# Kernel tuning notes

Hardware: AMD Instinct MI355X
Metric: run time of the kernel (lower is better)

Reference implementation:

```python
import jax, jax.numpy as jnp
import numpy as np

N, H, R, C = 50000, 16, 32, 8   # nodes, hidden, relations, classes
E = 1600000                      # edges (avg degree 32)


def setup_inputs() -> dict:
    key = jax.random.key(0)
    ks = jax.random.split(key, 6)
    edge_index = jax.random.randint(ks[0], (2, E), 0, N)
    edge_type = jax.random.randint(ks[1], (E,), 0, R)
    w1 = jax.random.normal(ks[2], (R, N, H), dtype=jnp.float32) * 0.05
    root1 = jax.random.normal(ks[3], (N, H), dtype=jnp.float32) * 0.05
    b1 = jnp.zeros((H,), jnp.float32)
    w2 = jax.random.normal(ks[4], (R, H, C), dtype=jnp.float32) * 0.05
    root2 = jax.random.normal(ks[5], (H, C), dtype=jnp.float32) * 0.05
    b2 = jnp.zeros((C,), jnp.float32)
    return {"edge_index": edge_index, "edge_type": edge_type,
            "w1": w1, "root1": root1, "b1": b1,
            "w2": w2, "root2": root2, "b2": b2}


def _rel_mean_agg(msgs, dst, edge_type, num_nodes, num_rel):
    """PyG RGCNConv aggregation: mean over edges within each (relation, target)
    pair, then sum over relations. msgs: [E, d] -> [num_nodes, d]."""
    seg = edge_type * num_nodes + dst                      # combined segment id
    tot = num_rel * num_nodes
    summed = jax.ops.segment_sum(msgs, seg, num_segments=tot)      # [R*N, d]
    cnt = jax.ops.segment_sum(jnp.ones((msgs.shape[0],), msgs.dtype), seg,
                              num_segments=tot)                    # [R*N]
    mean = summed / jnp.maximum(cnt, 1.0)[:, None]
    return mean.reshape(num_rel, num_nodes, -1).sum(axis=0)       # [N, d]


def reference(edge_index, edge_type, w1, root1, b1, w2, root2, b2):
    src, dst = edge_index[0], edge_index[1]
    # ---- layer 1: x = None -> message is weight row indexed by (rel, src)
    msgs1 = w1[edge_type, src]                             # [E, H] gather
    x = _rel_mean_agg(msgs1, dst, edge_type, N, R) + root1 + b1
    x = jax.nn.relu(x)
    # ---- layer 2: precompute per-relation transforms once: [R, N, C]
    xw = jnp.einsum('nh,rhc->rnc', x, w2)
    msgs2 = xw[edge_type, src]                             # [E, C] gather
    out = _rel_mean_agg(msgs2, dst, edge_type, N, R) + x @ root2 + b2
    return jax.nn.log_softmax(out, axis=1)
```

## Files before the change

### kernel.cpp

```cpp
#include <hip/hip_runtime.h>
#include <hip/hip_bf16.h>


constexpr int Nn = 50000;
constexpr int Hh = 16;
constexpr int Rr = 32;
constexpr int Cc = 8;
constexpr int Ee = 1600000;
constexpr int CHUNK = 4096;
constexpr int NC = (Ee + CHUNK - 1) / CHUNK;
constexpr int DSH = 7;
constexpr unsigned DLOWM = 127u;
constexpr int NBKT = (Nn + 127) / 128;
constexpr int K1 = (NC + 255) / 256;
constexpr int K2 = (NBKT + 255) / 256;
constexpr int KE = CHUNK / 256;
constexpr int SCAP = 5120;

__device__ __forceinline__ float b2f(__hip_bfloat16 v) { return __bfloat162float(v); }
__device__ __forceinline__ float bs2f(unsigned short u) {
    return __uint_as_float(((unsigned)u) << 16);
}

__global__ __launch_bounds__(256) void histA_kernel(const int* __restrict__ dst,
                                                    unsigned* __restrict__ H,
                                                    const unsigned short* __restrict__ w1s,
                                                    int* __restrict__ flag) {
    __shared__ unsigned hb[NBKT];
    int c = blockIdx.x, tid = threadIdx.x;
    if (c == 0 && tid == 0) {
        int hits = 0;
        for (int i = 0; i < 64; ++i) {
            unsigned short u = w1s[2 * i];
            int e = (u >> 7) & 0xFF;
            if (e >= 100 && e <= 130) ++hits;
        }
        *flag = (hits >= 32) ? 1 : 0;
    }
    for (int i = tid; i < NBKT; i += 256) hb[i] = 0;
    __syncthreads();
    int base = c * CHUNK;
    int n = min(CHUNK, Ee - base);
    for (int i = tid; i < n; i += 256)
        atomicAdd(&hb[((unsigned)dst[base + i]) >> DSH], 1u);
    __syncthreads();
    for (int i = tid; i < NBKT; i += 256) H[(size_t)c * NBKT + i] = hb[i];
}

__global__ __launch_bounds__(256) void scanB1_kernel(unsigned* __restrict__ H,
                                                     unsigned* __restrict__ bt) {
    __shared__ int lsum[4];
    int b = blockIdx.x, t = threadIdx.x, lane = t & 63, wv = t >> 6;
    int c0 = t * K1;
    int v[K1];
#pragma unroll
    for (int j = 0; j < K1; ++j) {
        int c = c0 + j;
        v[j] = (c < NC) ? (int)H[(size_t)c * NBKT + b] : 0;
    }
    int tot = 0;
#pragma unroll
    for (int j = 0; j < K1; ++j) { int tmp = v[j]; v[j] = tot; tot += tmp; }
    int s = tot;
#pragma unroll
    for (int o = 1; o < 64; o <<= 1) { int u = __shfl_up(s, o, 64); if (lane >= o) s += u; }
    if (lane == 63) lsum[wv] = s;
    __syncthreads();
    int basev = 0;
    for (int j = 0; j < wv; ++j) basev += lsum[j];
    int excl = basev + s - tot;
#pragma unroll
    for (int j = 0; j < K1; ++j) {
        int c = c0 + j;
        if (c < NC) H[(size_t)c * NBKT + b] = (unsigned)(excl + v[j]);
    }
    if (t == 255) bt[b] = (unsigned)(basev + s);
}

__global__ __launch_bounds__(256) void scanB2_kernel(const unsigned* __restrict__ bt,
                                                     unsigned* __restrict__ rbase) {
    __shared__ int lsum[4];
    int t = threadIdx.x, lane = t & 63, wv = t >> 6;
    int c0 = t * K2;
    int v[K2];
#pragma unroll
    for (int j = 0; j < K2; ++j) {
        int c = c0 + j;
        v[j] = (c < NBKT) ? (int)bt[c] : 0;
    }
    int tot = 0;
#pragma unroll
    for (int j = 0; j < K2; ++j) { int tmp = v[j]; v[j] = tot; tot += tmp; }
    int s = tot;
#pragma unroll
    for (int o = 1; o < 64; o <<= 1) { int u = __shfl_up(s, o, 64); if (lane >= o) s += u; }
    if (lane == 63) lsum[wv] = s;
    __syncthreads();
    int basev = 0;
    for (int j = 0; j < wv; ++j) basev += lsum[j];
    int excl = basev + s - tot;
#pragma unroll
    for (int j = 0; j < K2; ++j) {
        int c = c0 + j;
        if (c < NBKT) rbase[c] = (unsigned)(excl + v[j]);
    }
    if (t == 255) rbase[NBKT] = (unsigned)(basev + s);
}

__global__ __launch_bounds__(256) void scatC_kernel(const int* __restrict__ src,
                                                    const int* __restrict__ dst,
                                                    const int* __restrict__ et,
                                                    const unsigned* __restrict__ H,
                                                    const unsigned* __restrict__ rbase,
                                                    unsigned* __restrict__ rec) {
    __shared__ unsigned bb[NBKT];
    __shared__ unsigned hb[NBKT];
    __shared__ unsigned stg[CHUNK];
    __shared__ unsigned short bkt16[CHUNK];
    __shared__ int lsum[4];
    int c = blockIdx.x, t = threadIdx.x, lane = t & 63, wv = t >> 6;
    for (int i = t; i < NBKT; i += 256) {
        bb[i] = H[(size_t)c * NBKT + i] + rbase[i];
        hb[i] = 0;
    }
    __syncthreads();
    int base = c * CHUNK;
    int n = min(CHUNK, Ee - base);
    unsigned rcd[KE]; unsigned short bk[KE], rk[KE];
#pragma unroll
    for (int k = 0; k < KE; ++k) {
        int i = t + k * 256;
        if (i < n) {
            int e = base + i;
            unsigned d = (unsigned)dst[e];
            rcd[k] = (unsigned)src[e] | ((unsigned)et[e] << 16) | ((d & DLOWM) << 21);
            unsigned bkt = d >> DSH;
            bk[k] = (unsigned short)bkt;
            rk[k] = (unsigned short)atomicAdd(&hb[bkt], 1u);
        }
    }
    __syncthreads();
    {
        int c0 = t * 2;
        int v0 = (c0 < NBKT) ? (int)hb[c0] : 0;
        int v1 = (c0 + 1 < NBKT) ? (int)hb[c0 + 1] : 0;
        int pair = v0 + v1, s = pair;
#pragma unroll
        for (int o = 1; o < 64; o <<= 1) { int u = __shfl_up(s, o, 64); if (lane >= o) s += u; }
        if (lane == 63) lsum[wv] = s;
        __syncthreads();
        int basev = 0;
        for (int j = 0; j < wv; ++j) basev += lsum[j];
        int excl = basev + s - pair;
        if (c0 < NBKT) hb[c0] = (unsigned)excl;
        if (c0 + 1 < NBKT) hb[c0 + 1] = (unsigned)(excl + v0);
    }
    __syncthreads();
#pragma unroll
    for (int k = 0; k < KE; ++k) {
        int i = t + k * 256;
        if (i < n) {
            unsigned slot = hb[bk[k]] + rk[k];
            stg[slot] = rcd[k];
            bkt16[slot] = bk[k];
        }
    }
    __syncthreads();
    for (int i = t; i < n; i += 256) {
        unsigned b = bkt16[i];
        rec[bb[b] + (i - hb[b])] = stg[i];
    }
}

__global__ __launch_bounds__(256) void sortDl1_kernel(const unsigned* __restrict__ rec,
                                                      const unsigned* __restrict__ rbase,
                                                      unsigned* __restrict__ sorted,
                                                      int* __restrict__ offs,
                                                      const void* __restrict__ w1,
                                                      const void* __restrict__ root1,
                                                      const void* __restrict__ b1,
                                                      const int* __restrict__ flag,
                                                      float* __restrict__ x) {
    __shared__ unsigned cnt[128 * 33];
    __shared__ unsigned sb[128 * 33];
    __shared__ unsigned stg[SCAP];
    __shared__ unsigned dstart[129];
    __shared__ int l2s[2];
    int b = blockIdx.x, t = threadIdx.x, lane = t & 63, wv = t >> 6;
    for (int i = t; i < 128 * 33; i += 256) cnt[i] = 0;
    __syncthreads();
    unsigned rb = rbase[b], re = rbase[b + 1];
    int n = (int)(re - rb);
    for (int i = t; i < n; i += 256) {
        unsigned w = rec[rb + i];
        atomicAdd(&cnt[((w >> 21) & 127u) * 33 + ((w >> 16) & 31u)], 1u);
    }
    __syncthreads();
    int deg = 0;
    if (t < 128) {
#pragma unroll
        for (int r = 0; r < 32; ++r) {
            unsigned cc = cnt[t * 33 + r];
            sb[t * 33 + r] = (unsigned)deg;
            deg += (int)cc;
        }
    }
    int s = deg;
#pragma unroll
    for (int o = 1; o < 64; o <<= 1) { int u = __shfl_up(s, o, 64); if (lane >= o) s += u; }
    if (lane == 63 && wv < 2) l2s[wv] = s;
    __syncthreads();
    if (t < 128) {
        int excl = s - deg + (wv == 1 ? l2s[0] : 0);
        dstart[t] = (unsigned)excl;
        if (t == 127) dstart[128] = (unsigned)(excl + deg);
        int d = b * 128 + t;
        if (d <= Nn) offs[d] = (int)(rb + (unsigned)excl);
#pragma unroll
        for (int r = 0; r < 32; ++r) sb[t * 33 + r] += (unsigned)excl;
    }
    __syncthreads();
    for (int i = t; i < n; i += 256) {
        unsigned w = rec[rb + i];
        unsigned dlow = (w >> 21) & 127u, rel = (w >> 16) & 31u, sv = w & 0xFFFFu;
        int cell = (int)dlow * 33 + (int)rel;
        unsigned pos = atomicAdd(&sb[cell], 1u);
        unsigned cc = cnt[cell];
        if (cc > 2047u) cc = 2047u;
        stg[pos] = sv | (rel << 16) | (cc << 21);
    }
    __syncthreads();
    for (int i = t; i < n; i += 256) sorted[rb + i] = stg[i];
    int isbf = *flag;
    int ep = lane >> 2, hp = lane & 3;
    for (int j = 0; j < 32; ++j) {
        int dl = wv * 32 + j;
        int d = b * 128 + dl;
        if (d >= Nn) break;
        int s0 = (int)dstart[dl], s1 = (int)dstart[dl + 1];
        float a0 = 0.f, a1 = 0.f, a2 = 0.f, a3 = 0.f;
        if (isbf) {
            for (int i = s0 + ep; i < s1; i += 16) {
                unsigned p = stg[i];
                int ct = p >> 21, rel = (p >> 16) & 31, sv = p & 0xFFFF;
                float inv = __builtin_amdgcn_rcpf((float)ct);
                ushort4 v = ((const ushort4*)w1)[((size_t)rel * Nn + sv) * 4 + hp];
                a0 += inv * bs2f(v.x); a1 += inv * bs2f(v.y);
                a2 += inv * bs2f(v.z); a3 += inv * bs2f(v.w);
            }
        } else {
            for (int i = s0 + ep; i < s1; i += 16) {
                unsigned p = stg[i];
                int ct = p >> 21, rel = (p >> 16) & 31, sv = p & 0xFFFF;
                float inv = __builtin_amdgcn_rcpf((float)ct);
                float4 v = ((const float4*)w1)[((size_t)rel * Nn + sv) * 4 + hp];
                a0 += inv * v.x; a1 += inv * v.y; a2 += inv * v.z; a3 += inv * v.w;
            }
        }
#pragma unroll
        for (int o = 4; o < 64; o <<= 1) {
            a0 += __shfl_xor(a0, o, 64);
            a1 += __shfl_xor(a1, o, 64);
            a2 += __shfl_xor(a2, o, 64);
            a3 += __shfl_xor(a3, o, 64);
        }
        if (ep == 0) {
            float r0, r1, r2, r3, bb0, bb1, bb2, bb3;
            if (isbf) {
                ushort4 rv = ((const ushort4*)root1)[(size_t)d * 4 + hp];
                ushort4 bv = ((const ushort4*)b1)[hp];
                r0 = bs2f(rv.x); r1 = bs2f(rv.y); r2 = bs2f(rv.z); r3 = bs2f(rv.w);
                bb0 = bs2f(bv.x); bb1 = bs2f(bv.y); bb2 = bs2f(bv.z); bb3 = bs2f(bv.w);
            } else {
                float4 rv = ((const float4*)root1)[(size_t)d * 4 + hp];
                float4 bv = ((const float4*)b1)[hp];
                r0 = rv.x; r1 = rv.y; r2 = rv.z; r3 = rv.w;
                bb0 = bv.x; bb1 = bv.y; bb2 = bv.z; bb3 = bv.w;
            }
            float v0 = a0 + r0 + bb0, v1 = a1 + r1 + bb1;
            float v2 = a2 + r2 + bb2, v3 = a3 + r3 + bb3;
            *(float4*)(x + (size_t)d * Hh + hp * 4) =
                make_float4(v0 > 0.f ? v0 : 0.f, v1 > 0.f ? v1 : 0.f,
                            v2 > 0.f ? v2 : 0.f, v3 > 0.f ? v3 : 0.f);
        }
    }
}

__global__ __launch_bounds__(256) void l2_kernel(const unsigned* __restrict__ sorted,
                                                 const int* __restrict__ offs,
                                                 const float* __restrict__ x,
                                                 const void* __restrict__ w2,
                                                 const void* __restrict__ root2,
                                                 const void* __restrict__ b2v,
                                                 const int* __restrict__ flag,
                                                 void* __restrict__ out) {
    __shared__ float w2s[32 * 132];
    __shared__ float rsh[128];
    __shared__ float b2sh[8];
    int tid = threadIdx.x, w = tid >> 6, lane = tid & 63;
    int isbf = *flag;
    {
        int r = tid >> 3, cc = tid & 7;
        if (isbf) {
            const __hip_bfloat16* W = (const __hip_bfloat16*)w2 + r * 128 + cc;
#pragma unroll
            for (int h = 0; h < 16; ++h) w2s[r * 132 + cc * 16 + h] = b2f(W[h * 8]);
        } else {
            const float* W = (const float*)w2 + r * 128 + cc;
#pragma unroll
            for (int h = 0; h < 16; ++h) w2s[r * 132 + cc * 16 + h] = W[h * 8];
        }
    }
    if (tid < 128) rsh[tid] = isbf ? b2f(((const __hip_bfloat16*)root2)[tid])
                                   : ((const float*)root2)[tid];
    if (tid < 8)   b2sh[tid] = isbf ? b2f(((const __hip_bfloat16*)b2v)[tid])
                                    : ((const float*)b2v)[tid];
    __syncthreads();
    int ep = lane >> 3, c = lane & 7;
    int d = blockIdx.x * 4 + w;
    int off = offs[d], deg = offs[d + 1] - off;
    float acc = 0.0f;
    for (int i0 = 0; i0 < deg; i0 += 8) {
        int i = i0 + ep;
        if (i < deg) {
            unsigned p = sorted[off + i];
            int cnt = p >> 21, rel = (p >> 16) & 31, s = p & 0xFFFF;
            float inv = __builtin_amdgcn_rcpf((float)cnt);
            const float4* xr = (const float4*)(x + (size_t)s * Hh);
            float4 x0 = xr[0], x1 = xr[1], x2 = xr[2], x3 = xr[3];
            const float4* wv = (const float4*)(w2s + rel * 132 + c * 16);
            float4 w0 = wv[0], w1v = wv[1], w2v = wv[2], w3 = wv[3];
            float dot = x0.x*w0.x + x0.y*w0.y + x0.z*w0.z + x0.w*w0.w
                      + x1.x*w1v.x + x1.y*w1v.y + x1.z*w1v.z + x1.w*w1v.w
                      + x2.x*w2v.x + x2.y*w2v.y + x2.z*w2v.z + x2.w*w2v.w
                      + x3.x*w3.x + x3.y*w3.y + x3.z*w3.z + x3.w*w3.w;
            acc += inv * dot;
        }
    }
    acc += __shfl_xor(acc, 8, 64);
    acc += __shfl_xor(acc, 16, 64);
    acc += __shfl_xor(acc, 32, 64);
    if (ep == 0) {
        const float4* xr = (const float4*)(x + (size_t)d * Hh);
        float4 x0 = xr[0], x1 = xr[1], x2 = xr[2], x3 = xr[3];
        float xv[16] = {x0.x,x0.y,x0.z,x0.w, x1.x,x1.y,x1.z,x1.w,
                        x2.x,x2.y,x2.z,x2.w, x3.x,x3.y,x3.z,x3.w};
        float v = acc + b2sh[c];
#pragma unroll
        for (int h = 0; h < 16; ++h) v += xv[h] * rsh[h * 8 + c];
        float m = v;
#pragma unroll
        for (int o = 1; o < 8; o <<= 1) m = fmaxf(m, __shfl_xor(m, o, 8));
        float ssum = __expf(v - m);
#pragma unroll
        for (int o = 1; o < 8; o <<= 1) ssum += __shfl_xor(ssum, o, 8);
        float res = v - m - __logf(ssum);
        if (isbf) ((__hip_bfloat16*)out)[(size_t)d * Cc + c] = __float2bfloat16(res);
        else      ((float*)out)[(size_t)d * Cc + c] = res;
    }
}

extern "C" void kernel_launch(void* const* d_in, const int* in_sizes, int n_in,
                              void* d_out, int out_size, void* d_ws, size_t ws_size,
                              hipStream_t stream) {
    const int* edge_index = (const int*)d_in[0];
    const int* src = edge_index;
    const int* dst = edge_index + Ee;
    const int* et  = (const int*)d_in[1];
    const void* w1    = d_in[2];
    const void* root1 = d_in[3];
    const void* b1    = d_in[4];
    const void* w2    = d_in[5];
    const void* root2 = d_in[6];
    const void* b2    = d_in[7];

    unsigned* rec    = (unsigned*)d_ws;
    unsigned* sorted = rec + Ee;
    float*    x      = (float*)(sorted + Ee);
    unsigned* H      = (unsigned*)(x + (size_t)Nn * Hh);
    unsigned* bt     = H + (size_t)NC * NBKT;
    unsigned* rbase  = bt + NBKT;
    int* offs        = (int*)(rbase + NBKT + 1);
    int* flag        = offs + Nn + 4;

    histA_kernel<<<NC, 256, 0, stream>>>(dst, H, (const unsigned short*)w1, flag);
    scanB1_kernel<<<NBKT, 256, 0, stream>>>(H, bt);
    scanB2_kernel<<<1, 256, 0, stream>>>(bt, rbase);
    scatC_kernel<<<NC, 256, 0, stream>>>(src, dst, et, H, rbase, rec);
    sortDl1_kernel<<<NBKT, 256, 0, stream>>>(rec, rbase, sorted, offs,
                                             w1, root1, b1, flag, x);
    l2_kernel<<<Nn / 4, 256, 0, stream>>>(sorted, offs, x, w2, root2, b2, flag, d_out);
}
```

Measured before the change: 316.4 us.

## Replace per-destination sort with bucketed LDS atomic accumulation for both layers

```diff
diff --git a/kernel.cpp b/kernel.cpp
--- a/kernel.cpp
+++ b/kernel.cpp
@@ -9,18 +9,20 @@
 constexpr int Ee = 1600000;
 constexpr int CHUNK = 4096;
 constexpr int NC = (Ee + CHUNK - 1) / CHUNK;
-constexpr int DSH = 7;
-constexpr unsigned DLOWM = 127u;
-constexpr int NBKT = (Nn + 127) / 128;
+constexpr int DSH = 6;
+constexpr unsigned DLOWM = 63u;
+constexpr int NBKT = (Nn + 63) / 64;
 constexpr int K1 = (NC + 255) / 256;
 constexpr int K2 = (NBKT + 255) / 256;
+constexpr int KH = 4;
 constexpr int KE = CHUNK / 256;
-constexpr int SCAP = 5120;
-
-__device__ __forceinline__ float b2f(__hip_bfloat16 v) { return __bfloat162float(v); }
+constexpr unsigned SENT = 0xFFFFFFFFu;
+
 __device__ __forceinline__ float bs2f(unsigned short u) {
     return __uint_as_float(((unsigned)u) << 16);
 }
+__device__ __forceinline__ float blo(unsigned u) { return __uint_as_float(u << 16); }
+__device__ __forceinline__ float bhi(unsigned u) { return __uint_as_float(u & 0xFFFF0000u); }
 
 __global__ __launch_bounds__(256) void histA_kernel(const int* __restrict__ dst,
                                                     unsigned* __restrict__ H,
@@ -141,19 +143,29 @@
     }
     __syncthreads();
     {
-        int c0 = t * 2;
-        int v0 = (c0 < NBKT) ? (int)hb[c0] : 0;
-        int v1 = (c0 + 1 < NBKT) ? (int)hb[c0 + 1] : 0;
-        int pair = v0 + v1, s = pair;
+        int c0 = t * KH;
+        int v[KH];
+#pragma unroll
+        for (int j = 0; j < KH; ++j) {
+            int cc = c0 + j;
+            v[j] = (cc < NBKT) ? (int)hb[cc] : 0;
+        }
+        int tot = 0;
+#pragma unroll
+        for (int j = 0; j < KH; ++j) { int tmp = v[j]; v[j] = tot; tot += tmp; }
+        int s = tot;
 #pragma unroll
         for (int o = 1; o < 64; o <<= 1) { int u = __shfl_up(s, o, 64); if (lane >= o) s += u; }
         if (lane == 63) lsum[wv] = s;
         __syncthreads();
         int basev = 0;
         for (int j = 0; j < wv; ++j) basev += lsum[j];
-        int excl = basev + s - pair;
-        if (c0 < NBKT) hb[c0] = (unsigned)excl;
-        if (c0 + 1 < NBKT) hb[c0 + 1] = (unsigned)(excl + v0);
+        int excl = basev + s - tot;
+#pragma unroll
+        for (int j = 0; j < KH; ++j) {
+            int cc = c0 + j;
+            if (cc < NBKT) hb[cc] = (unsigned)(excl + v[j]);
+        }
     }
     __syncthreads();
 #pragma unroll
@@ -172,191 +184,248 @@
     }
 }
 
-__global__ __launch_bounds__(256) void sortDl1_kernel(const unsigned* __restrict__ rec,
-                                                      const unsigned* __restrict__ rbase,
-                                                      unsigned* __restrict__ sorted,
-                                                      int* __restrict__ offs,
-                                                      const void* __restrict__ w1,
-                                                      const void* __restrict__ root1,
-                                                      const void* __restrict__ b1,
-                                                      const int* __restrict__ flag,
-                                                      float* __restrict__ x) {
-    __shared__ unsigned cnt[128 * 33];
-    __shared__ unsigned sb[128 * 33];
-    __shared__ unsigned stg[SCAP];
-    __shared__ unsigned dstart[129];
-    __shared__ int l2s[2];
-    int b = blockIdx.x, t = threadIdx.x, lane = t & 63, wv = t >> 6;
-    for (int i = t; i < 128 * 33; i += 256) cnt[i] = 0;
+__global__ __launch_bounds__(256) void l1B_kernel(const unsigned* __restrict__ rec,
+                                                  const unsigned* __restrict__ rbase,
+                                                  const void* __restrict__ w1,
+                                                  const void* __restrict__ root1,
+                                                  const void* __restrict__ b1,
+                                                  const int* __restrict__ flag,
+                                                  float* __restrict__ x) {
+    __shared__ unsigned cnt[64 * 33];
+    __shared__ float xacc[64 * 17];
+    int b = blockIdx.x, t = threadIdx.x;
+    for (int i = t; i < 64 * 33; i += 256) cnt[i] = 0;
+    for (int i = t; i < 64 * 17; i += 256) xacc[i] = 0.f;
     __syncthreads();
     unsigned rb = rbase[b], re = rbase[b + 1];
     int n = (int)(re - rb);
     for (int i = t; i < n; i += 256) {
         unsigned w = rec[rb + i];
-        atomicAdd(&cnt[((w >> 21) & 127u) * 33 + ((w >> 16) & 31u)], 1u);
-    }
-    __syncthreads();
-    int deg = 0;
-    if (t < 128) {
-#pragma unroll
-        for (int r = 0; r < 32; ++r) {
-            unsigned cc = cnt[t * 33 + r];
-            sb[t * 33 + r] = (unsigned)deg;
-            deg += (int)cc;
-        }
-    }
-    int s = deg;
-#pragma unroll
-    for (int o = 1; o < 64; o <<= 1) { int u = __shfl_up(s, o, 64); if (lane >= o) s += u; }
-    if (lane == 63 && wv < 2) l2s[wv] = s;
-    __syncthreads();
-    if (t < 128) {
-        int excl = s - deg + (wv == 1 ? l2s[0] : 0);
-        dstart[t] = (unsigned)excl;
-        if (t == 127) dstart[128] = (unsigned)(excl + deg);
-        int d = b * 128 + t;
-        if (d <= Nn) offs[d] = (int)(rb + (unsigned)excl);
-#pragma unroll
-        for (int r = 0; r < 32; ++r) sb[t * 33 + r] += (unsigned)excl;
-    }
-    __syncthreads();
-    for (int i = t; i < n; i += 256) {
-        unsigned w = rec[rb + i];
-        unsigned dlow = (w >> 21) & 127u, rel = (w >> 16) & 31u, sv = w & 0xFFFFu;
-        int cell = (int)dlow * 33 + (int)rel;
-        unsigned pos = atomicAdd(&sb[cell], 1u);
-        unsigned cc = cnt[cell];
-        if (cc > 2047u) cc = 2047u;
-        stg[pos] = sv | (rel << 16) | (cc << 21);
-    }
-    __syncthreads();
-    for (int i = t; i < n; i += 256) sorted[rb + i] = stg[i];
+        atomicAdd(&cnt[((w >> 21) & 63u) * 33 + ((w >> 16) & 31u)], 1u);
+    }
+    __syncthreads();
     int isbf = *flag;
-    int ep = lane >> 2, hp = lane & 3;
-    for (int j = 0; j < 32; ++j) {
-        int dl = wv * 32 + j;
-        int d = b * 128 + dl;
-        if (d >= Nn) break;
-        int s0 = (int)dstart[dl], s1 = (int)dstart[dl + 1];
-        float a0 = 0.f, a1 = 0.f, a2 = 0.f, a3 = 0.f;
-        if (isbf) {
-            for (int i = s0 + ep; i < s1; i += 16) {
-                unsigned p = stg[i];
-                int ct = p >> 21, rel = (p >> 16) & 31, sv = p & 0xFFFF;
-                float inv = __builtin_amdgcn_rcpf((float)ct);
-                ushort4 v = ((const ushort4*)w1)[((size_t)rel * Nn + sv) * 4 + hp];
-                a0 += inv * bs2f(v.x); a1 += inv * bs2f(v.y);
-                a2 += inv * bs2f(v.z); a3 += inv * bs2f(v.w);
-            }
-        } else {
-            for (int i = s0 + ep; i < s1; i += 16) {
-                unsigned p = stg[i];
-                int ct = p >> 21, rel = (p >> 16) & 31, sv = p & 0xFFFF;
-                float inv = __builtin_amdgcn_rcpf((float)ct);
-                float4 v = ((const float4*)w1)[((size_t)rel * Nn + sv) * 4 + hp];
-                a0 += inv * v.x; a1 += inv * v.y; a2 += inv * v.z; a3 += inv * v.w;
-            }
-        }
-#pragma unroll
-        for (int o = 4; o < 64; o <<= 1) {
-            a0 += __shfl_xor(a0, o, 64);
-            a1 += __shfl_xor(a1, o, 64);
-            a2 += __shfl_xor(a2, o, 64);
-            a3 += __shfl_xor(a3, o, 64);
-        }
-        if (ep == 0) {
-            float r0, r1, r2, r3, bb0, bb1, bb2, bb3;
+    if (isbf) {
+        for (int i0 = 0; i0 < n; i0 += 1024) {
+            unsigned wv[4]; uint4 ga[4], gb[4];
+#pragma unroll
+            for (int k = 0; k < 4; ++k) {
+                int idx = i0 + t + k * 256;
+                wv[k] = (idx < n) ? rec[rb + idx] : SENT;
+            }
+#pragma unroll
+            for (int k = 0; k < 4; ++k) {
+                if (wv[k] != SENT) {
+                    int rel = (wv[k] >> 16) & 31, sv = wv[k] & 0xFFFF;
+                    const uint4* p = (const uint4*)w1 + ((size_t)rel * Nn + sv) * 2;
+                    ga[k] = p[0]; gb[k] = p[1];
+                }
+            }
+#pragma unroll
+            for (int k = 0; k < 4; ++k) {
+                if (wv[k] != SENT) {
+                    int dlow = (wv[k] >> 21) & 63, rel = (wv[k] >> 16) & 31;
+                    float inv = __builtin_amdgcn_rcpf((float)cnt[dlow * 33 + rel]);
+                    unsigned uu[8] = {ga[k].x, ga[k].y, ga[k].z, ga[k].w,
+                                      gb[k].x, gb[k].y, gb[k].z, gb[k].w};
+                    float* xr = &xacc[dlow * 17];
+#pragma unroll
+                    for (int q = 0; q < 8; ++q) {
+                        atomicAdd(&xr[2 * q],     inv * blo(uu[q]));
+                        atomicAdd(&xr[2 * q + 1], inv * bhi(uu[q]));
+                    }
+                }
+            }
+        }
+    } else {
+        for (int i0 = 0; i0 < n; i0 += 512) {
+            unsigned wv[2]; float4 g[2][4];
+#pragma unroll
+            for (int k = 0; k < 2; ++k) {
+                int idx = i0 + t + k * 256;
+                wv[k] = (idx < n) ? rec[rb + idx] : SENT;
+            }
+#pragma unroll
+            for (int k = 0; k < 2; ++k) {
+                if (wv[k] != SENT) {
+                    int rel = (wv[k] >> 16) & 31, sv = wv[k] & 0xFFFF;
+                    const float4* p = (const float4*)w1 + ((size_t)rel * Nn + sv) * 4;
+                    g[k][0] = p[0]; g[k][1] = p[1]; g[k][2] = p[2]; g[k][3] = p[3];
+                }
+            }
+#pragma unroll
+            for (int k = 0; k < 2; ++k) {
+                if (wv[k] != SENT) {
+                    int dlow = (wv[k] >> 21) & 63, rel = (wv[k] >> 16) & 31;
+                    float inv = __builtin_amdgcn_rcpf((float)cnt[dlow * 33 + rel]);
+                    const float* gv = (const float*)&g[k][0];
+                    float* xr = &xacc[dlow * 17];
+#pragma unroll
+                    for (int h = 0; h < 16; ++h) atomicAdd(&xr[h], inv * gv[h]);
+                }
+            }
+        }
+    }
+    __syncthreads();
+    if (t < 64) {
+        int d = b * 64 + t;
+        if (d < Nn) {
+            float vv[16];
+#pragma unroll
+            for (int h = 0; h < 16; ++h) vv[h] = xacc[t * 17 + h];
             if (isbf) {
-                ushort4 rv = ((const ushort4*)root1)[(size_t)d * 4 + hp];
-                ushort4 bv = ((const ushort4*)b1)[hp];
-                r0 = bs2f(rv.x); r1 = bs2f(rv.y); r2 = bs2f(rv.z); r3 = bs2f(rv.w);
-                bb0 = bs2f(bv.x); bb1 = bs2f(bv.y); bb2 = bs2f(bv.z); bb3 = bs2f(bv.w);
+                const uint4* rp = (const uint4*)root1 + (size_t)d * 2;
+                uint4 r0 = rp[0], r1 = rp[1];
+                const uint4* bp = (const uint4*)b1;
+                uint4 b0 = bp[0], b1w = bp[1];
+                unsigned ru[8] = {r0.x, r0.y, r0.z, r0.w, r1.x, r1.y, r1.z, r1.w};
+                unsigned bu[8] = {b0.x, b0.y, b0.z, b0.w, b1w.x, b1w.y, b1w.z, b1w.w};
+#pragma unroll
+                for (int q = 0; q < 8; ++q) {
+                    vv[2 * q]     += blo(ru[q]) + blo(bu[q]);
+                    vv[2 * q + 1] += bhi(ru[q]) + bhi(bu[q]);
+                }
             } else {
-                float4 rv = ((const float4*)root1)[(size_t)d * 4 + hp];
-                float4 bv = ((const float4*)b1)[hp];
-                r0 = rv.x; r1 = rv.y; r2 = rv.z; r3 = rv.w;
-                bb0 = bv.x; bb1 = bv.y; bb2 = bv.z; bb3 = bv.w;
-            }
-            float v0 = a0 + r0 + bb0, v1 = a1 + r1 + bb1;
-            float v2 = a2 + r2 + bb2, v3 = a3 + r3 + bb3;
-            *(float4*)(x + (size_t)d * Hh + hp * 4) =
-                make_float4(v0 > 0.f ? v0 : 0.f, v1 > 0.f ? v1 : 0.f,
-                            v2 > 0.f ? v2 : 0.f, v3 > 0.f ? v3 : 0.f);
-        }
-    }
-}
-
-__global__ __launch_bounds__(256) void l2_kernel(const unsigned* __restrict__ sorted,
-                                                 const int* __restrict__ offs,
-                                                 const float* __restrict__ x,
-                                                 const void* __restrict__ w2,
-                                                 const void* __restrict__ root2,
-                                                 const void* __restrict__ b2v,
-                                                 const int* __restrict__ flag,
-                                                 void* __restrict__ out) {
+                const float4* rp = (const float4*)root1 + (size_t)d * 4;
+                const float4* bp = (const float4*)b1;
+                float4 rr[4] = {rp[0], rp[1], rp[2], rp[3]};
+                float4 bb4[4] = {bp[0], bp[1], bp[2], bp[3]};
+                const float* rf = (const float*)rr;
+                const float* bf = (const float*)bb4;
+#pragma unroll
+                for (int h = 0; h < 16; ++h) vv[h] += rf[h] + bf[h];
+            }
+            float4* xo = (float4*)(x + (size_t)d * Hh);
+#pragma unroll
+            for (int q = 0; q < 4; ++q) {
+                float v0 = vv[4 * q],     v1 = vv[4 * q + 1];
+                float v2 = vv[4 * q + 2], v3 = vv[4 * q + 3];
+                xo[q] = make_float4(v0 > 0.f ? v0 : 0.f, v1 > 0.f ? v1 : 0.f,
+                                    v2 > 0.f ? v2 : 0.f, v3 > 0.f ? v3 : 0.f);
+            }
+        }
+    }
+}
+
+__global__ __launch_bounds__(256) void l2B_kernel(const unsigned* __restrict__ rec,
+                                                  const unsigned* __restrict__ rbase,
+                                                  const float* __restrict__ x,
+                                                  const void* __restrict__ w2,
+                                                  const void* __restrict__ root2,
+                                                  const void* __restrict__ b2v,
+                                                  const int* __restrict__ flag,
+                                                  void* __restrict__ out) {
     __shared__ float w2s[32 * 132];
     __shared__ float rsh[128];
     __shared__ float b2sh[8];
-    int tid = threadIdx.x, w = tid >> 6, lane = tid & 63;
+    __shared__ unsigned cnt[64 * 33];
+    __shared__ float oacc[64 * 9];
+    int b = blockIdx.x, t = threadIdx.x;
     int isbf = *flag;
     {
-        int r = tid >> 3, cc = tid & 7;
+        int r = t >> 3, cc = t & 7;
         if (isbf) {
             const __hip_bfloat16* W = (const __hip_bfloat16*)w2 + r * 128 + cc;
 #pragma unroll
-            for (int h = 0; h < 16; ++h) w2s[r * 132 + cc * 16 + h] = b2f(W[h * 8]);
+            for (int h = 0; h < 16; ++h)
+                w2s[r * 132 + cc * 16 + h] = __bfloat162float(W[h * 8]);
         } else {
             const float* W = (const float*)w2 + r * 128 + cc;
 #pragma unroll
             for (int h = 0; h < 16; ++h) w2s[r * 132 + cc * 16 + h] = W[h * 8];
         }
     }
-    if (tid < 128) rsh[tid] = isbf ? b2f(((const __hip_bfloat16*)root2)[tid])
-                                   : ((const float*)root2)[tid];
-    if (tid < 8)   b2sh[tid] = isbf ? b2f(((const __hip_bfloat16*)b2v)[tid])
-                                    : ((const float*)b2v)[tid];
-    __syncthreads();
-    int ep = lane >> 3, c = lane & 7;
-    int d = blockIdx.x * 4 + w;
-    int off = offs[d], deg = offs[d + 1] - off;
-    float acc = 0.0f;
-    for (int i0 = 0; i0 < deg; i0 += 8) {
-        int i = i0 + ep;
-        if (i < deg) {
-            unsigned p = sorted[off + i];
-            int cnt = p >> 21, rel = (p >> 16) & 31, s = p & 0xFFFF;
-            float inv = __builtin_amdgcn_rcpf((float)cnt);
-            const float4* xr = (const float4*)(x + (size_t)s * Hh);
+    if (t < 128) rsh[t] = isbf ? __bfloat162float(((const __hip_bfloat16*)root2)[t])
+                               : ((const float*)root2)[t];
+    if (t < 8)   b2sh[t] = isbf ? __bfloat162float(((const __hip_bfloat16*)b2v)[t])
+                                : ((const float*)b2v)[t];
+    for (int i = t; i < 64 * 33; i += 256) cnt[i] = 0;
+    for (int i = t; i < 64 * 9; i += 256) oacc[i] = 0.f;
+    __syncthreads();
+    unsigned rb = rbase[b], re = rbase[b + 1];
+    int n = (int)(re - rb);
+    for (int i = t; i < n; i += 256) {
+        unsigned w = rec[rb + i];
+        atomicAdd(&cnt[((w >> 21) & 63u) * 33 + ((w >> 16) & 31u)], 1u);
+    }
+    __syncthreads();
+    for (int i0 = 0; i0 < n; i0 += 512) {
+        unsigned wv[2]; float4 xg[2][4];
+#pragma unroll
+        for (int k = 0; k < 2; ++k) {
+            int idx = i0 + t + k * 256;
+            wv[k] = (idx < n) ? rec[rb + idx] : SENT;
+        }
+#pragma unroll
+        for (int k = 0; k < 2; ++k) {
+            if (wv[k] != SENT) {
+                int sv = wv[k] & 0xFFFF;
+                const float4* xr = (const float4*)(x + (size_t)sv * Hh);
+                xg[k][0] = xr[0]; xg[k][1] = xr[1]; xg[k][2] = xr[2]; xg[k][3] = xr[3];
+            }
+        }
+#pragma unroll
+        for (int k = 0; k < 2; ++k) {
+            if (wv[k] != SENT) {
+                int dlow = (wv[k] >> 21) & 63, rel = (wv[k] >> 16) & 31;
+                float inv = __builtin_amdgcn_rcpf((float)cnt[dlow * 33 + rel]);
+                const float* wvp = &w2s[rel * 132];
+                float4 x0 = xg[k][0], x1 = xg[k][1], x2 = xg[k][2], x3 = xg[k][3];
+#pragma unroll
+                for (int c = 0; c < 8; ++c) {
+                    const float4* wc = (const float4*)(wvp + c * 16);
+                    float4 w0 = wc[0], w1v = wc[1], w2v = wc[2], w3 = wc[3];
+                    float dot = x0.x*w0.x + x0.y*w0.y + x0.z*w0.z + x0.w*w0.w
+                              + x1.x*w1v.x + x1.y*w1v.y + x1.z*w1v.z + x1.w*w1v.w
+                              + x2.x*w2v.x + x2.y*w2v.y + x2.z*w2v.z + x2.w*w2v.w
+                              + x3.x*w3.x + x3.y*w3.y + x3.z*w3.z + x3.w*w3.w;
+                    atomicAdd(&oacc[dlow * 9 + c], inv * dot);
+                }
+            }
+        }
+    }
+    __syncthreads();
+    if (t < 64) {
+        int d = b * 64 + t;
+        if (d < Nn) {
+            const float4* xr = (const float4*)(x + (size_t)d * Hh);
             float4 x0 = xr[0], x1 = xr[1], x2 = xr[2], x3 = xr[3];
-            const float4* wv = (const float4*)(w2s + rel * 132 + c * 16);
-            float4 w0 = wv[0], w1v = wv[1], w2v = wv[2], w3 = wv[3];
-            float dot = x0.x*w0.x + x0.y*w0.y + x0.z*w0.z + x0.w*w0.w
-                      + x1.x*w1v.x + x1.y*w1v.y + x1.z*w1v.z + x1.w*w1v.w
-                      + x2.x*w2v.x + x2.y*w2v.y + x2.z*w2v.z + x2.w*w2v.w
-                      + x3.x*w3.x + x3.y*w3.y + x3.z*w3.z + x3.w*w3.w;
-            acc += inv * dot;
-        }
-    }
-    acc += __shfl_xor(acc, 8, 64);
-    acc += __shfl_xor(acc, 16, 64);
-    acc += __shfl_xor(acc, 32, 64);
-    if (ep == 0) {
-        const float4* xr = (const float4*)(x + (size_t)d * Hh);
-        float4 x0 = xr[0], x1 = xr[1], x2 = xr[2], x3 = xr[3];
-        float xv[16] = {x0.x,x0.y,x0.z,x0.w, x1.x,x1.y,x1.z,x1.w,
-                        x2.x,x2.y,x2.z,x2.w, x3.x,x3.y,x3.z,x3.w};
-        float v = acc + b2sh[c];
-#pragma unroll
-        for (int h = 0; h < 16; ++h) v += xv[h] * rsh[h * 8 + c];
-        float m = v;
-#pragma unroll
-        for (int o = 1; o < 8; o <<= 1) m = fmaxf(m, __shfl_xor(m, o, 8));
-        float ssum = __expf(v - m);
-#pragma unroll
-        for (int o = 1; o < 8; o <<= 1) ssum += __shfl_xor(ssum, o, 8);
-        float res = v - m - __logf(ssum);
-        if (isbf) ((__hip_bfloat16*)out)[(size_t)d * Cc + c] = __float2bfloat16(res);
-        else      ((float*)out)[(size_t)d * Cc + c] = res;
+            float xv[16] = {x0.x,x0.y,x0.z,x0.w, x1.x,x1.y,x1.z,x1.w,
+                            x2.x,x2.y,x2.z,x2.w, x3.x,x3.y,x3.z,x3.w};
+            float v[8];
+#pragma unroll
+            for (int c = 0; c < 8; ++c) v[c] = oacc[t * 9 + c] + b2sh[c];
+#pragma unroll
+            for (int h = 0; h < 16; ++h) {
+                float xh = xv[h];
+#pragma unroll
+                for (int c = 0; c < 8; ++c) v[c] += xh * rsh[h * 8 + c];
+            }
+            float m = v[0];
+#pragma unroll
+            for (int c = 1; c < 8; ++c) m = fmaxf(m, v[c]);
+            float ssum = 0.f;
+#pragma unroll
+            for (int c = 0; c < 8; ++c) ssum += __expf(v[c] - m);
+            float lg = m + __logf(ssum);
+            if (isbf) {
+                unsigned pw[4];
+#pragma unroll
+                for (int q = 0; q < 4; ++q) {
+                    __hip_bfloat16 h0 = __float2bfloat16(v[2 * q] - lg);
+                    __hip_bfloat16 h1 = __float2bfloat16(v[2 * q + 1] - lg);
+                    unsigned u0 = *reinterpret_cast<unsigned short*>(&h0);
+                    unsigned u1 = *reinterpret_cast<unsigned short*>(&h1);
+                    pw[q] = u0 | (u1 << 16);
+                }
+                *(uint4*)((unsigned short*)out + (size_t)d * Cc) =
+                    make_uint4(pw[0], pw[1], pw[2], pw[3]);
+            } else {
+                float4* op = (float4*)((float*)out + (size_t)d * Cc);
+                op[0] = make_float4(v[0] - lg, v[1] - lg, v[2] - lg, v[3] - lg);
+                op[1] = make_float4(v[4] - lg, v[5] - lg, v[6] - lg, v[7] - lg);
+            }
+        }
     }
 }
 
@@ -374,20 +443,17 @@
     const void* root2 = d_in[6];
     const void* b2    = d_in[7];
 
-    unsigned* rec    = (unsigned*)d_ws;
-    unsigned* sorted = rec + Ee;
-    float*    x      = (float*)(sorted + Ee);
-    unsigned* H      = (unsigned*)(x + (size_t)Nn * Hh);
-    unsigned* bt     = H + (size_t)NC * NBKT;
-    unsigned* rbase  = bt + NBKT;
-    int* offs        = (int*)(rbase + NBKT + 1);
-    int* flag        = offs + Nn + 4;
+    unsigned* rec   = (unsigned*)d_ws;
+    float*    x     = (float*)(rec + Ee);
+    unsigned* H     = (unsigned*)(x + (size_t)Nn * Hh);
+    unsigned* bt    = H + (size_t)NC * NBKT;
+    unsigned* rbase = bt + NBKT;
+    int* flag       = (int*)(rbase + NBKT + 1);
 
     histA_kernel<<<NC, 256, 0, stream>>>(dst, H, (const unsigned short*)w1, flag);
     scanB1_kernel<<<NBKT, 256, 0, stream>>>(H, bt);
     scanB2_kernel<<<1, 256, 0, stream>>>(bt, rbase);
     scatC_kernel<<<NC, 256, 0, stream>>>(src, dst, et, H, rbase, rec);
-    sortDl1_kernel<<<NBKT, 256, 0, stream>>>(rec, rbase, sorted, offs,
-                                             w1, root1, b1, flag, x);
-    l2_kernel<<<Nn / 4, 256, 0, stream>>>(sorted, offs, x, w2, root2, b2, flag, d_out);
-}
+    l1B_kernel<<<NBKT, 256, 0, stream>>>(rec, rbase, w1, root1, b1, flag, x);
+    l2B_kernel<<<NBKT, 256, 0, stream>>>(rec, rbase, x, w2, root2, b2, flag, d_out);
+}
```

After: 463.4 us. 46.5% more time.
